# Performance work log

Measured on AMD Instinct MI355X. Metric: run time of the kernel, lower is better.

The kernel has to match this reference:

```python
import jax, jax.numpy as jnp
import numpy as np

B, N, C = 4, 32768, 256
H, CH, M = 8, 64, 64  # heads, dim_head, slice_num
INNER = H * CH


def setup_inputs() -> dict:
    key = jax.random.key(0)
    ks = jax.random.split(key, 16)
    s = lambda fan_in: 1.0 / np.sqrt(fan_in)
    return {
        "x": jax.random.normal(ks[0], (B, N, C), jnp.float32),
        "x_cross": jax.random.normal(ks[1], (B, N, C), jnp.float32),
        "Wfx": jax.random.normal(ks[2], (C, INNER), jnp.float32) * s(C),
        "bfx": jnp.zeros((INNER,), jnp.float32),
        "Wx": jax.random.normal(ks[3], (C, INNER), jnp.float32) * s(C),
        "bx": jnp.zeros((INNER,), jnp.float32),
        "Wslice": jax.random.normal(ks[4], (CH, M), jnp.float32) * s(CH),
        "bslice": jnp.zeros((M,), jnp.float32),
        "temperature": jnp.ones((1, H, 1, 1), jnp.float32) * 0.5,
        "Wq": jax.random.normal(ks[5], (CH, CH), jnp.float32) * s(CH),
        "Wk": jax.random.normal(ks[6], (CH, CH), jnp.float32) * s(CH),
        "Wv": jax.random.normal(ks[7], (CH, CH), jnp.float32) * s(CH),
        "Wo": jax.random.normal(ks[8], (INNER, C), jnp.float32) * s(INNER),
        "bo": jnp.zeros((C,), jnp.float32),
    }


def _split_heads(y):
    # [B, N, H*CH] -> [B, H, N, CH]
    return y.reshape(B, N, H, CH).transpose(0, 2, 1, 3)


def _project_token(x, Wfx, bfx, Wx, bx, Wslice, bslice, temperature):
    fx_mid = _split_heads(x @ Wfx + bfx)  # bhnc
    x_mid = _split_heads(x @ Wx + bx)     # bhnc
    temp = jnp.clip(temperature, 0.1, 5.0)
    logits = (x_mid @ Wslice + bslice) / temp  # b h n M
    sw = jax.nn.softmax(logits, axis=-1)
    sw = sw / (sw.sum(axis=2, keepdims=True) + 1e-5)  # normalize over N per slice
    token = jnp.einsum('bhnc,bhng->bhgc', fx_mid, sw)  # b h M CH
    return token, sw


def reference(x, x_cross, Wfx, bfx, Wx, bx, Wslice, bslice, temperature,
              Wq, Wk, Wv, Wo, bo):
    token, sw = _project_token(x, Wfx, bfx, Wx, bx, Wslice, bslice, temperature)
    token_c, _ = _project_token(x_cross, Wfx, bfx, Wx, bx, Wslice, bslice, temperature)

    q = token @ Wq    # b h M CH
    k = token_c @ Wk
    v = token_c @ Wv
    scale = CH ** -0.5
    attn = jax.nn.softmax(jnp.einsum('bhgc,bhmc->bhgm', q, k) * scale, axis=-1)
    out_tok = jnp.einsum('bhgm,bhmc->bhgc', attn, v)  # b h M CH

    out_x = jnp.einsum('bhgc,bhng->bhnc', out_tok, sw)  # b h N CH
    out_x = out_x.transpose(0, 2, 1, 3).reshape(B, N, INNER)
    return out_x @ Wo + bo
```

## Files before the change

### kernel.cpp

```cpp
#include <hip/hip_runtime.h>
#include <math.h>

constexpr int Bc = 4, Nc = 32768, Cc = 256, Hc = 8, CHc = 64, Mc = 64, INNERc = 512;

typedef _Float16 h8 __attribute__((ext_vector_type(8)));
typedef _Float16 h4 __attribute__((ext_vector_type(4)));
typedef float f32x4 __attribute__((ext_vector_type(4)));

__device__ __forceinline__ void fma4x4(float acc[4][4], const float4 a, const float4 b) {
  acc[0][0] += a.x*b.x; acc[0][1] += a.x*b.y; acc[0][2] += a.x*b.z; acc[0][3] += a.x*b.w;
  acc[1][0] += a.y*b.x; acc[1][1] += a.y*b.y; acc[1][2] += a.y*b.z; acc[1][3] += a.y*b.w;
  acc[2][0] += a.z*b.x; acc[2][1] += a.z*b.y; acc[2][2] += a.z*b.z; acc[2][3] += a.z*b.w;
  acc[3][0] += a.w*b.x; acc[3][1] += a.w*b.y; acc[3][2] += a.w*b.z; acc[3][3] += a.w*b.w;
}

__global__ __launch_bounds__(256, 2)
void project_token_kernel(const float* __restrict__ Xx, const float* __restrict__ Xc,
                          const float* __restrict__ Wfx, const float* __restrict__ bfx,
                          const float* __restrict__ Wx, const float* __restrict__ bx,
                          const float* __restrict__ Wsl, const float* __restrict__ bsl,
                          const float* __restrict__ temp,
                          float* __restrict__ TUx, float* __restrict__ TUc,
                          float* __restrict__ Ssx, float* __restrict__ Ssc)
{
  __shared__ __align__(16) _Float16 Xst[2][2][64][40];
  __shared__ __align__(16) _Float16 FXT[2][64][72];
  __shared__ __align__(16) _Float16 XMT[2][64][72];
  __shared__ __align__(16) float Sred[16][64];

  const int t = threadIdx.x;
  const int chunk = blockIdx.x, h = blockIdx.y, bz = blockIdx.z;
  const int b = bz & 3;
  const float* X = (bz < 4) ? Xx : Xc;
  float* TU   = (bz < 4) ? TUx : TUc;
  float* Ssum = (bz < 4) ? Ssx : Ssc;
  const int bh = b * Hc + h, colBase = h * 64;
  const int w = t >> 6, l = t & 63, lg = l >> 4, lr = l & 15;
  const int stok = t >> 2, sc8 = (t & 3) << 3;

  const float invt = 1.0f / fminf(fmaxf(temp[h], 0.1f), 5.0f);

  const float* Wsrc = (w < 2) ? Wfx : Wx;
  const float* bsrc = (w < 2) ? bfx : bx;
  const int wcb = colBase + ((w & 1) << 5);
  h8 wfh[8][2], wfl[8][2];
  float biasv[2];
#pragma unroll
  for (int n = 0; n < 2; ++n) {
    const int col = wcb + (n << 4) + lr;
    biasv[n] = bsrc[col];
#pragma unroll
    for (int ks = 0; ks < 8; ++ks)
#pragma unroll
      for (int j = 0; j < 8; ++j) {
        const float v = Wsrc[(long)((ks << 5) + (lg << 3) + j) * INNERc + col];
        const _Float16 hi = (_Float16)v;
        wfh[ks][n][j] = hi;
        wfl[ks][n][j] = (_Float16)(v - (float)hi);
      }
  }
  h8 wslh[2][4], wsll[2][4];
#pragma unroll
  for (int ks = 0; ks < 2; ++ks)
#pragma unroll
    for (int n = 0; n < 4; ++n)
#pragma unroll
      for (int j = 0; j < 8; ++j) {
        const float v = Wsl[((ks << 5) + (lg << 3) + j) * 64 + (n << 4) + lr];
        const _Float16 hi = (_Float16)v;
        wslh[ks][n][j] = hi;
        wsll[ks][n][j] = (_Float16)(v - (float)hi);
      }
  float bs_n[4];
#pragma unroll
  for (int n = 0; n < 4; ++n) bs_n[n] = bsl[(n << 4) + lr];

  f32x4 tuacc[4] = {};
  float sregn[4] = {};

  for (int tile = 0; tile < 32; ++tile) {
    const int n0 = chunk * 2048 + tile * 64;
    const long xRow = ((long)(b * Nc + n0 + stok)) * Cc + sc8;

    f32x4 acc[4][2] = {};
    {
      const float4 xa = *(const float4*)&X[xRow];
      const float4 xb = *(const float4*)&X[xRow + 4];
      const float va[8] = {xa.x, xa.y, xa.z, xa.w, xb.x, xb.y, xb.z, xb.w};
      h8 hv, lv;
#pragma unroll
      for (int j = 0; j < 8; ++j) {
        const _Float16 hi = (_Float16)va[j];
        hv[j] = hi; lv[j] = (_Float16)(va[j] - (float)hi);
      }
      *(h8*)&Xst[0][0][stok][sc8] = hv;
      *(h8*)&Xst[0][1][stok][sc8] = lv;
    }
#pragma unroll
    for (int ks = 0; ks < 8; ++ks) {
      const int cb = ks & 1;
      __syncthreads();
      float4 xa, xb;
      if (ks < 7) {
        xa = *(const float4*)&X[xRow + ((ks + 1) << 5)];
        xb = *(const float4*)&X[xRow + ((ks + 1) << 5) + 4];
      }
#pragma unroll
      for (int m = 0; m < 4; ++m) {
        const h8 ah = *(const h8*)&Xst[cb][0][(m << 4) + lr][lg << 3];
        const h8 al = *(const h8*)&Xst[cb][1][(m << 4) + lr][lg << 3];
#pragma unroll
        for (int n = 0; n < 2; ++n) {
          acc[m][n] = __builtin_amdgcn_mfma_f32_16x16x32_f16(ah, wfh[ks][n], acc[m][n], 0, 0, 0);
          acc[m][n] = __builtin_amdgcn_mfma_f32_16x16x32_f16(al, wfh[ks][n], acc[m][n], 0, 0, 0);
          acc[m][n] = __builtin_amdgcn_mfma_f32_16x16x32_f16(ah, wfl[ks][n], acc[m][n], 0, 0, 0);
        }
      }
      if (ks < 7) {
        const float va[8] = {xa.x, xa.y, xa.z, xa.w, xb.x, xb.y, xb.z, xb.w};
        h8 hv, lv;
#pragma unroll
        for (int j = 0; j < 8; ++j) {
          const _Float16 hi = (_Float16)va[j];
          hv[j] = hi; lv[j] = (_Float16)(va[j] - (float)hi);
        }
        *(h8*)&Xst[cb ^ 1][0][stok][sc8] = hv;
        *(h8*)&Xst[cb ^ 1][1][stok][sc8] = lv;
      }
    }

    if (w < 2) {
#pragma unroll
      for (int m = 0; m < 4; ++m)
#pragma unroll
        for (int n = 0; n < 2; ++n) {
          const int c = ((w & 1) << 5) + (n << 4) + lr;
          const int tokb = (m << 4) + (lg << 2);
          h4 hv, lv;
#pragma unroll
          for (int i = 0; i < 4; ++i) {
            const float v = acc[m][n][i] + biasv[n];
            const _Float16 hi = (_Float16)v;
            hv[i] = hi; lv[i] = (_Float16)(v - (float)hi);
          }
          *(h4*)&FXT[0][c][tokb] = hv;
          *(h4*)&FXT[1][c][tokb] = lv;
        }
    } else {
#pragma unroll
      for (int m = 0; m < 4; ++m)
#pragma unroll
        for (int n = 0; n < 2; ++n) {
          const int c = ((w & 1) << 5) + (n << 4) + lr;
#pragma unroll
          for (int i = 0; i < 4; ++i) {
            const float v = acc[m][n][i] + biasv[n];
            const _Float16 hi = (_Float16)v;
            XMT[0][(m << 4) + (lg << 2) + i][c] = hi;
            XMT[1][(m << 4) + (lg << 2) + i][c] = (_Float16)(v - (float)hi);
          }
        }
    }
    __syncthreads();

    f32x4 lga[4] = {};
#pragma unroll
    for (int ks = 0; ks < 2; ++ks) {
      const h8 ah = *(const h8*)&XMT[0][(w << 4) + lr][(ks << 5) + (lg << 3)];
      const h8 al = *(const h8*)&XMT[1][(w << 4) + lr][(ks << 5) + (lg << 3)];
#pragma unroll
      for (int n = 0; n < 4; ++n) {
        lga[n] = __builtin_amdgcn_mfma_f32_16x16x32_f16(ah, wslh[ks][n], lga[n], 0, 0, 0);
        lga[n] = __builtin_amdgcn_mfma_f32_16x16x32_f16(al, wslh[ks][n], lga[n], 0, 0, 0);
        lga[n] = __builtin_amdgcn_mfma_f32_16x16x32_f16(ah, wsll[ks][n], lga[n], 0, 0, 0);
      }
    }
    __syncthreads();

    float sw[4][4];
#pragma unroll
    for (int i = 0; i < 4; ++i) {
      float mx = -1e30f;
#pragma unroll
      for (int n = 0; n < 4; ++n) {
        const float lv = (lga[n][i] + bs_n[n]) * invt;
        sw[n][i] = lv; mx = fmaxf(mx, lv);
      }
      for (int d = 1; d < 16; d <<= 1) mx = fmaxf(mx, __shfl_xor(mx, d));
      float s = 0.f;
#pragma unroll
      for (int n = 0; n < 4; ++n) { sw[n][i] = __expf(sw[n][i] - mx); s += sw[n][i]; }
      for (int d = 1; d < 16; d <<= 1) s += __shfl_xor(s, d);
      const float inv = 1.0f / s;
#pragma unroll
      for (int n = 0; n < 4; ++n) { sw[n][i] *= inv; sregn[n] += sw[n][i]; }
    }
#pragma unroll
    for (int n = 0; n < 4; ++n) {
      h4 hv, lv;
#pragma unroll
      for (int i = 0; i < 4; ++i) {
        const _Float16 hi = (_Float16)sw[n][i];
        hv[i] = hi; lv[i] = (_Float16)(sw[n][i] - (float)hi);
      }
      *(h4*)&XMT[0][(n << 4) + lr][(w << 4) + (lg << 2)] = hv;
      *(h4*)&XMT[1][(n << 4) + lr][(w << 4) + (lg << 2)] = lv;
    }
    __syncthreads();

#pragma unroll
    for (int ks = 0; ks < 2; ++ks) {
      const h8 ah = *(const h8*)&XMT[0][(w << 4) + lr][(ks << 5) + (lg << 3)];
      const h8 al = *(const h8*)&XMT[1][(w << 4) + lr][(ks << 5) + (lg << 3)];
#pragma unroll
      for (int n = 0; n < 4; ++n) {
        const h8 bhv = *(const h8*)&FXT[0][(n << 4) + lr][(ks << 5) + (lg << 3)];
        const h8 blv = *(const h8*)&FXT[1][(n << 4) + lr][(ks << 5) + (lg << 3)];
        tuacc[n] = __builtin_amdgcn_mfma_f32_16x16x32_f16(ah, bhv, tuacc[n], 0, 0, 0);
        tuacc[n] = __builtin_amdgcn_mfma_f32_16x16x32_f16(al, bhv, tuacc[n], 0, 0, 0);
        tuacc[n] = __builtin_amdgcn_mfma_f32_16x16x32_f16(ah, blv, tuacc[n], 0, 0, 0);
      }
    }
  }

#pragma unroll
  for (int n = 0; n < 4; ++n)
#pragma unroll
    for (int i = 0; i < 4; ++i)
      atomicAdd(&TU[((long)bh * 64 + (w << 4) + (lg << 2) + i) * 64 + (n << 4) + lr],
                tuacc[n][i]);

  __syncthreads();
#pragma unroll
  for (int n = 0; n < 4; ++n) Sred[(w << 2) + lg][(n << 4) + lr] = sregn[n];
  __syncthreads();
  if (t < 64) {
    float s = 0.f;
    for (int r = 0; r < 16; ++r) s += Sred[r][t];
    atomicAdd(&Ssum[bh * 64 + t], s);
  }
}

__global__ __launch_bounds__(64)
void att_kernel(const float* __restrict__ TUx, const float* __restrict__ TUc,
                const float* __restrict__ Sx, const float* __restrict__ Sc,
                const float* __restrict__ Wq, const float* __restrict__ Wk,
                const float* __restrict__ Wv, float* __restrict__ OT)
{
  __shared__ __align__(16) float W[64][68];
  __shared__ __align__(16) float Km[64][68];
  __shared__ __align__(16) float Vm[64][68];
  const int bh = blockIdx.x;
  const int g  = threadIdx.x;
  const float invc = 1.0f / (Sc[bh * 64 + g] + 1e-5f);
  const float invx = 1.0f / (Sx[bh * 64 + g] + 1e-5f);

  for (int i = 0; i < 64; ++i) W[i][g] = Wk[i * 64 + g];
  __syncthreads();
  {
    float4 a[16]; for (int j = 0; j < 16; ++j) a[j] = make_float4(0,0,0,0);
    for (int c = 0; c < 64; ++c) {
      const float tc = TUc[((long)bh * 64 + g) * 64 + c] * invc;
#pragma unroll
      for (int j = 0; j < 16; ++j) {
        const float4 w4 = *(const float4*)&W[c][j << 2];
        a[j].x += tc*w4.x; a[j].y += tc*w4.y; a[j].z += tc*w4.z; a[j].w += tc*w4.w;
      }
    }
    for (int j = 0; j < 16; ++j) *(float4*)&Km[g][j << 2] = a[j];
  }
  __syncthreads();
  for (int i = 0; i < 64; ++i) W[i][g] = Wv[i * 64 + g];
  __syncthreads();
  {
    float4 a[16]; for (int j = 0; j < 16; ++j) a[j] = make_float4(0,0,0,0);
    for (int c = 0; c < 64; ++c) {
      const float tc = TUc[((long)bh * 64 + g) * 64 + c] * invc;
#pragma unroll
      for (int j = 0; j < 16; ++j) {
        const float4 w4 = *(const float4*)&W[c][j << 2];
        a[j].x += tc*w4.x; a[j].y += tc*w4.y; a[j].z += tc*w4.z; a[j].w += tc*w4.w;
      }
    }
    for (int j = 0; j < 16; ++j) *(float4*)&Vm[g][j << 2] = a[j];
  }
  __syncthreads();
  for (int i = 0; i < 64; ++i) W[i][g] = Wq[i * 64 + g];
  __syncthreads();
  float4 qa[16]; for (int j = 0; j < 16; ++j) qa[j] = make_float4(0,0,0,0);
  for (int c = 0; c < 64; ++c) {
    const float tq = TUx[((long)bh * 64 + g) * 64 + c] * invx;
#pragma unroll
    for (int j = 0; j < 16; ++j) {
      const float4 w4 = *(const float4*)&W[c][j << 2];
      qa[j].x += tq*w4.x; qa[j].y += tq*w4.y; qa[j].z += tq*w4.z; qa[j].w += tq*w4.w;
    }
  }
  __syncthreads();
  float (*Am)[68] = W;
  float mx = -1e30f;
  for (int m = 0; m < 64; ++m) {
    float s = 0.f;
#pragma unroll
    for (int j = 0; j < 16; ++j) {
      const float4 k4 = *(const float4*)&Km[m][j << 2];
      s += qa[j].x*k4.x + qa[j].y*k4.y + qa[j].z*k4.z + qa[j].w*k4.w;
    }
    s *= 0.125f;
    Am[m][g] = s;
    mx = fmaxf(mx, s);
  }
  float sum = 0.f;
  for (int m = 0; m < 64; ++m) { const float ev = __expf(Am[m][g] - mx); Am[m][g] = ev; sum += ev; }
  float4 oa[16]; for (int j = 0; j < 16; ++j) oa[j] = make_float4(0,0,0,0);
  for (int m = 0; m < 64; ++m) {
    const float am = Am[m][g];
#pragma unroll
    for (int j = 0; j < 16; ++j) {
      const float4 v4 = *(const float4*)&Vm[m][j << 2];
      oa[j].x += am*v4.x; oa[j].y += am*v4.y; oa[j].z += am*v4.z; oa[j].w += am*v4.w;
    }
  }
  const float so = invx / sum;
#pragma unroll
  for (int j = 0; j < 16; ++j) {
    OT[((long)bh * 64 + ((j<<2)+0)) * 64 + g] = oa[j].x * so;
    OT[((long)bh * 64 + ((j<<2)+1)) * 64 + g] = oa[j].y * so;
    OT[((long)bh * 64 + ((j<<2)+2)) * 64 + g] = oa[j].z * so;
    OT[((long)bh * 64 + ((j<<2)+3)) * 64 + g] = oa[j].w * so;
  }
}

__global__ __launch_bounds__(256)
void wofold_kernel(const float* __restrict__ OT, const float* __restrict__ Wo,
                   _Float16* __restrict__ WoTth, _Float16* __restrict__ WoTtl)
{
  __shared__ __align__(16) float OTs[64][68];
  __shared__ __align__(16) float Wos[64][68];
  const int t = threadIdx.x, tx = t & 15, ty = t >> 4;
  const int cot = blockIdx.x * 64, bh = blockIdx.y, h = bh & 7;
#pragma unroll
  for (int rep = 0; rep < 4; ++rep) {
    const int v = t + rep * 256, r = v >> 4, q4 = (v & 15) << 2;
    *(float4*)&OTs[r][q4] = *(const float4*)&OT[((long)bh * 64 + r) * 64 + q4];
    *(float4*)&Wos[r][q4] = *(const float4*)&Wo[(long)(h * 64 + r) * 256 + cot + q4];
  }
  __syncthreads();
  float acc[4][4] = {};
#pragma unroll
  for (int k = 0; k < 64; ++k) {
    const float4 a = *(const float4*)&OTs[k][ty << 2];
    fma4x4(acc, a, *(const float4*)&Wos[k][tx << 2]);
  }
#pragma unroll
  for (int i = 0; i < 4; ++i)
#pragma unroll
    for (int j = 0; j < 4; ++j) {
      const float v = acc[i][j];
      const _Float16 hi = (_Float16)v;
      const long o = ((long)bh * 256 + cot + (tx<<2)+j) * 64 + (ty<<2)+i;
      WoTth[o] = hi;
      WoTtl[o] = (_Float16)(v - (float)hi);
    }
}

__global__ __launch_bounds__(256)
void wxprep_kernel(const float* __restrict__ Wx, _Float16* __restrict__ Wxth,
                   _Float16* __restrict__ Wxtl)
{
  __shared__ __align__(16) float Ls[64][68];
  const int t = threadIdx.x;
  const int k0 = blockIdx.x * 64, c0 = blockIdx.y * 64;
  const int r = t >> 4, c4 = (t & 15) << 2;
#pragma unroll
  for (int rr = 0; rr < 4; ++rr)
    *(float4*)&Ls[(rr<<4)+r][c4] = *(const float4*)&Wx[(long)(k0+(rr<<4)+r) * 512 + c0 + c4];
  __syncthreads();
  const int cl = t >> 2, kq = (t & 3) << 4;
  h8 hv0, hv1, lv0, lv1;
#pragma unroll
  for (int kk = 0; kk < 8; ++kk) {
    float v = Ls[kq+kk][cl];
    _Float16 hi = (_Float16)v;
    hv0[kk] = hi; lv0[kk] = (_Float16)(v - (float)hi);
    v = Ls[kq+8+kk][cl];
    hi = (_Float16)v;
    hv1[kk] = hi; lv1[kk] = (_Float16)(v - (float)hi);
  }
  const long o = (long)(c0 + cl) * 256 + k0 + kq;
  *(h8*)&Wxth[o]     = hv0; *(h8*)&Wxth[o + 8] = hv1;
  *(h8*)&Wxtl[o]     = lv0; *(h8*)&Wxtl[o + 8] = lv1;
}

__global__ __launch_bounds__(256, 1)
void outx_kernel(const float* __restrict__ X, const _Float16* __restrict__ Wxth,
                 const _Float16* __restrict__ Wxtl, const float* __restrict__ bx,
                 const float* __restrict__ Wsl, const float* __restrict__ bsl,
                 const float* __restrict__ temp,
                 const _Float16* __restrict__ WoTth, const _Float16* __restrict__ WoTtl,
                 const float* __restrict__ bo, float* __restrict__ out)
{
  __shared__ __align__(16) _Float16 Xh[64][264];
  __shared__ __align__(16) _Float16 Xl[64][264];
  __shared__ __align__(16) _Float16 XMh[64][72];
  __shared__ __align__(16) _Float16 XMl[64][72];
  __shared__ __align__(16) float    Lg[64][68];

  const int t = threadIdx.x, tx = t & 15, ty = t >> 4;
  const int w = t >> 6, l = t & 63, lg = l >> 4, lr = l & 15;
  const int n0 = blockIdx.x * 64, b = blockIdx.y;
  const long xBase = ((long)b * Nc + n0) * Cc;

#pragma unroll
  for (int q = 0; q < 16; ++q) {
    const int row = (q << 2) + w, col = l << 2;
    const float4 v = *(const float4*)&X[xBase + (long)row * 256 + col];
    const float va[4] = {v.x, v.y, v.z, v.w};
    h4 hv, lv;
#pragma unroll
    for (int jj = 0; jj < 4; ++jj) {
      const _Float16 hi = (_Float16)va[jj];
      hv[jj] = hi; lv[jj] = (_Float16)(va[jj] - (float)hi);
    }
    *(h4*)&Xh[row][col] = hv;
    *(h4*)&Xl[row][col] = lv;
  }

  h8 wslh[2], wsll[2];
#pragma unroll
  for (int ks = 0; ks < 2; ++ks)
#pragma unroll
    for (int j = 0; j < 8; ++j) {
      const float v = Wsl[((ks << 5) + (lg << 3) + j) * 64 + (w << 4) + lr];
      const _Float16 hi = (_Float16)v;
      wslh[ks][j] = hi; wsll[ks][j] = (_Float16)(v - (float)hi);
    }
  const float bslv = bsl[(w << 4) + lr];

  f32x4 oacc[4][4] = {};

  __syncthreads();

  for (int h = 0; h < Hc; ++h) {
    h8 wxh[8], wxl[8];
    const long wxoff = (long)((h << 6) + (w << 4) + lr) * 256 + (lg << 3);
#pragma unroll
    for (int ks = 0; ks < 8; ++ks) {
      wxh[ks] = *(const h8*)&Wxth[wxoff + (ks << 5)];
      wxl[ks] = *(const h8*)&Wxtl[wxoff + (ks << 5)];
    }
    const float bxv = bx[(h << 6) + (w << 4) + lr];
    const float invt = 1.0f / fminf(fmaxf(temp[h], 0.1f), 5.0f);

    f32x4 xma[4] = {};
#pragma unroll
    for (int ks = 0; ks < 8; ++ks) {
#pragma unroll
      for (int m = 0; m < 4; ++m) {
        const h8 ah = *(const h8*)&Xh[(m << 4) + lr][(ks << 5) + (lg << 3)];
        const h8 al = *(const h8*)&Xl[(m << 4) + lr][(ks << 5) + (lg << 3)];
        xma[m] = __builtin_amdgcn_mfma_f32_16x16x32_f16(ah, wxh[ks], xma[m], 0, 0, 0);
        xma[m] = __builtin_amdgcn_mfma_f32_16x16x32_f16(al, wxh[ks], xma[m], 0, 0, 0);
        xma[m] = __builtin_amdgcn_mfma_f32_16x16x32_f16(ah, wxl[ks], xma[m], 0, 0, 0);
      }
    }
#pragma unroll
    for (int m = 0; m < 4; ++m)
#pragma unroll
      for (int i = 0; i < 4; ++i) {
        const float v = xma[m][i] + bxv;
        const _Float16 hi = (_Float16)v;
        XMh[(m << 4) + (lg << 2) + i][(w << 4) + lr] = hi;
        XMl[(m << 4) + (lg << 2) + i][(w << 4) + lr] = (_Float16)(v - (float)hi);
      }
    __syncthreads();

    const int bh = (b << 3) + h;
    h8 wth[4][2], wtl[4][2];
#pragma unroll
    for (int n = 0; n < 4; ++n)
#pragma unroll
      for (int ks = 0; ks < 2; ++ks) {
        const long o = ((long)(bh << 8) + (w << 6) + (n << 4) + lr) * 64 + (ks << 5) + (lg << 3);
        wth[n][ks] = *(const h8*)&WoTth[o];
        wtl[n][ks] = *(const h8*)&WoTtl[o];
      }

    f32x4 lga[4] = {};
#pragma unroll
    for (int ks = 0; ks < 2; ++ks)
#pragma unroll
      for (int m = 0; m < 4; ++m) {
        const h8 ah = *(const h8*)&XMh[(m << 4) + lr][(ks << 5) + (lg << 3)];
        const h8 al = *(const h8*)&XMl[(m << 4) + lr][(ks << 5) + (lg << 3)];
        lga[m] = __builtin_amdgcn_mfma_f32_16x16x32_f16(ah, wslh[ks], lga[m], 0, 0, 0);
        lga[m] = __builtin_amdgcn_mfma_f32_16x16x32_f16(al, wslh[ks], lga[m], 0, 0, 0);
        lga[m] = __builtin_amdgcn_mfma_f32_16x16x32_f16(ah, wsll[ks], lga[m], 0, 0, 0);
      }
#pragma unroll
    for (int m = 0; m < 4; ++m)
#pragma unroll
      for (int i = 0; i < 4; ++i)
        Lg[(m << 4) + (lg << 2) + i][(w << 4) + lr] = (lga[m][i] + bslv) * invt;
    __syncthreads();

    float e[4][4];
#pragma unroll
    for (int i = 0; i < 4; ++i) {
      const float4 lv4 = *(const float4*)&Lg[(ty << 2) + i][tx << 2];
      const float lrow[4] = {lv4.x, lv4.y, lv4.z, lv4.w};
      float mx = fmaxf(fmaxf(lrow[0], lrow[1]), fmaxf(lrow[2], lrow[3]));
      for (int d = 1; d < 16; d <<= 1) mx = fmaxf(mx, __shfl_xor(mx, d));
      float s = 0.f;
#pragma unroll
      for (int j = 0; j < 4; ++j) { e[i][j] = __expf(lrow[j] - mx); s += e[i][j]; }
      for (int d = 1; d < 16; d <<= 1) s += __shfl_xor(s, d);
      const float inv = 1.0f / s;
#pragma unroll
      for (int j = 0; j < 4; ++j) e[i][j] *= inv;
    }
#pragma unroll
    for (int i = 0; i < 4; ++i)
#pragma unroll
      for (int j = 0; j < 4; ++j) {
        const _Float16 hi = (_Float16)e[i][j];
        XMh[(ty << 2) + i][(tx << 2) + j] = hi;
        XMl[(ty << 2) + i][(tx << 2) + j] = (_Float16)(e[i][j] - (float)hi);
      }
    __syncthreads();

#pragma unroll
    for (int ks = 0; ks < 2; ++ks)
#pragma unroll
      for (int m = 0; m < 4; ++m) {
        const h8 ah = *(const h8*)&XMh[(m << 4) + lr][(ks << 5) + (lg << 3)];
        const h8 al = *(const h8*)&XMl[(m << 4) + lr][(ks << 5) + (lg << 3)];
#pragma unroll
        for (int n = 0; n < 4; ++n) {
          oacc[m][n] = __builtin_amdgcn_mfma_f32_16x16x32_f16(ah, wth[n][ks], oacc[m][n], 0, 0, 0);
          oacc[m][n] = __builtin_amdgcn_mfma_f32_16x16x32_f16(al, wth[n][ks], oacc[m][n], 0, 0, 0);
          oacc[m][n] = __builtin_amdgcn_mfma_f32_16x16x32_f16(ah, wtl[n][ks], oacc[m][n], 0, 0, 0);
        }
      }
    __syncthreads();
  }

#pragma unroll
  for (int n = 0; n < 4; ++n) {
    const float bov = bo[(w << 6) + (n << 4) + lr];
#pragma unroll
    for (int m = 0; m < 4; ++m)
#pragma unroll
      for (int i = 0; i < 4; ++i)
        out[((long)b * Nc + n0 + (m << 4) + (lg << 2) + i) * 256 + (w << 6) + (n << 4) + lr]
            = oacc[m][n][i] + bov;
  }
}

extern "C" void kernel_launch(void* const* d_in, const int* in_sizes, int n_in,
                              void* d_out, int out_size, void* d_ws, size_t ws_size,
                              hipStream_t stream)
{
  (void)in_sizes; (void)n_in; (void)out_size; (void)ws_size;
  const float* x    = (const float*)d_in[0];
  const float* xc   = (const float*)d_in[1];
  const float* Wfx  = (const float*)d_in[2];
  const float* bfx  = (const float*)d_in[3];
  const float* Wx   = (const float*)d_in[4];
  const float* bx   = (const float*)d_in[5];
  const float* Wsl  = (const float*)d_in[6];
  const float* bsl  = (const float*)d_in[7];
  const float* temp = (const float*)d_in[8];
  const float* Wq   = (const float*)d_in[9];
  const float* Wk   = (const float*)d_in[10];
  const float* Wv   = (const float*)d_in[11];
  const float* Wo   = (const float*)d_in[12];
  const float* bo   = (const float*)d_in[13];
  float* out = (float*)d_out;

  float* ws  = (float*)d_ws;
  float* Sx  = ws;
  float* Sc  = Sx + 2048;
  float* TUx = Sc + 2048;
  float* TUc = TUx + 131072;
  float* OT  = TUc + 131072;
  _Float16* WoTth = (_Float16*)(OT + 131072);
  _Float16* WoTtl = WoTth + 524288;
  _Float16* Wxth  = WoTtl + 524288;
  _Float16* Wxtl  = Wxth + 131072;

  hipMemsetAsync(Sx, 0, (size_t)(2 * 2048 + 2 * 131072) * sizeof(float), stream);

  wxprep_kernel<<<dim3(4, 8), 256, 0, stream>>>(Wx, Wxth, Wxtl);
  project_token_kernel<<<dim3(16, 8, 8), 256, 0, stream>>>(
      x, xc, Wfx, bfx, Wx, bx, Wsl, bsl, temp, TUx, TUc, Sx, Sc);
  att_kernel<<<dim3(32), dim3(64), 0, stream>>>(TUx, TUc, Sx, Sc, Wq, Wk, Wv, OT);
  wofold_kernel<<<dim3(4, 32), 256, 0, stream>>>(OT, Wo, WoTth, WoTtl);
  outx_kernel<<<dim3(512, 4), 256, 0, stream>>>(x, Wxth, Wxtl, bx, Wsl, bsl, temp, WoTth, WoTtl, bo, out);
}
```

Measured before the change: 1.551 ms.

## Precompute fp16 hi/lo planes of inputs and restructure outx softmax in registers

A new pre-pass splits x and x_cross into interleaved fp16 hi/lo planes. The x planes are stored in the output buffer as scratch, and the x_cross planes go into the workspace when it is large enough. project_token and outx then feed MFMA operands straight from these planes in global memory, instead of converting fp32 and staging through LDS on every pass. outx also keeps the slice logits and softmax in registers, dropping the Lg and X shared buffers, and asks for two blocks per CU. The cost is an extra full read/write pass over the inputs. It also relies on outx reading each block's own rows of out before overwriting them.

Result: slower. 2.727 ms (+75.8%).

```diff
diff --git a/kernel.cpp b/kernel.cpp
--- a/kernel.cpp
+++ b/kernel.cpp
@@ -14,8 +14,27 @@
   acc[3][0] += a.w*b.x; acc[3][1] += a.w*b.y; acc[3][2] += a.w*b.z; acc[3][3] += a.w*b.w;
 }
 
+__global__ __launch_bounds__(256)
+void xplanes_kernel(const float* __restrict__ src, _Float16* __restrict__ dst)
+{
+  const long idx = (long)blockIdx.x * 256 + threadIdx.x;
+  const long row = idx >> 5, oc = idx & 31;
+  const float4 a = *(const float4*)&src[(row << 8) + (oc << 3)];
+  const float4 b = *(const float4*)&src[(row << 8) + (oc << 3) + 4];
+  const float va[8] = {a.x, a.y, a.z, a.w, b.x, b.y, b.z, b.w};
+  h8 hv, lv;
+#pragma unroll
+  for (int j = 0; j < 8; ++j) {
+    const _Float16 hi = (_Float16)va[j];
+    hv[j] = hi; lv[j] = (_Float16)(va[j] - (float)hi);
+  }
+  *(h8*)&dst[(row << 9) + (oc << 4)]     = hv;
+  *(h8*)&dst[(row << 9) + (oc << 4) + 8] = lv;
+}
+
 __global__ __launch_bounds__(256, 2)
 void project_token_kernel(const float* __restrict__ Xx, const float* __restrict__ Xc,
+                          const _Float16* __restrict__ Xix, const _Float16* __restrict__ Xic,
                           const float* __restrict__ Wfx, const float* __restrict__ bfx,
                           const float* __restrict__ Wx, const float* __restrict__ bx,
                           const float* __restrict__ Wsl, const float* __restrict__ bsl,
@@ -26,12 +45,13 @@
   __shared__ __align__(16) _Float16 Xst[2][2][64][40];
   __shared__ __align__(16) _Float16 FXT[2][64][72];
   __shared__ __align__(16) _Float16 XMT[2][64][72];
-  __shared__ __align__(16) float Sred[16][64];
+  float (*Sred)[64] = (float(*)[64])&Xst[0][0][0][0];
 
   const int t = threadIdx.x;
   const int chunk = blockIdx.x, h = blockIdx.y, bz = blockIdx.z;
   const int b = bz & 3;
   const float* X = (bz < 4) ? Xx : Xc;
+  const _Float16* Xi = (bz < 4) ? Xix : Xic;
   float* TU   = (bz < 4) ? TUx : TUc;
   float* Ssum = (bz < 4) ? Ssx : Ssc;
   const int bh = b * Hc + h, colBase = h * 64;
@@ -80,43 +100,30 @@
 
   for (int tile = 0; tile < 32; ++tile) {
     const int n0 = chunk * 2048 + tile * 64;
-    const long xRow = ((long)(b * Nc + n0 + stok)) * Cc + sc8;
-
     f32x4 acc[4][2] = {};
-    {
-      const float4 xa = *(const float4*)&X[xRow];
-      const float4 xb = *(const float4*)&X[xRow + 4];
-      const float va[8] = {xa.x, xa.y, xa.z, xa.w, xb.x, xb.y, xb.z, xb.w};
-      h8 hv, lv;
-#pragma unroll
-      for (int j = 0; j < 8; ++j) {
-        const _Float16 hi = (_Float16)va[j];
-        hv[j] = hi; lv[j] = (_Float16)(va[j] - (float)hi);
-      }
-      *(h8*)&Xst[0][0][stok][sc8] = hv;
-      *(h8*)&Xst[0][1][stok][sc8] = lv;
-    }
-#pragma unroll
-    for (int ks = 0; ks < 8; ++ks) {
-      const int cb = ks & 1;
+
+    if (Xi) {
       __syncthreads();
-      float4 xa, xb;
-      if (ks < 7) {
-        xa = *(const float4*)&X[xRow + ((ks + 1) << 5)];
-        xb = *(const float4*)&X[xRow + ((ks + 1) << 5) + 4];
-      }
-#pragma unroll
-      for (int m = 0; m < 4; ++m) {
-        const h8 ah = *(const h8*)&Xst[cb][0][(m << 4) + lr][lg << 3];
-        const h8 al = *(const h8*)&Xst[cb][1][(m << 4) + lr][lg << 3];
-#pragma unroll
-        for (int n = 0; n < 2; ++n) {
-          acc[m][n] = __builtin_amdgcn_mfma_f32_16x16x32_f16(ah, wfh[ks][n], acc[m][n], 0, 0, 0);
-          acc[m][n] = __builtin_amdgcn_mfma_f32_16x16x32_f16(al, wfh[ks][n], acc[m][n], 0, 0, 0);
-          acc[m][n] = __builtin_amdgcn_mfma_f32_16x16x32_f16(ah, wfl[ks][n], acc[m][n], 0, 0, 0);
-        }
-      }
-      if (ks < 7) {
+      const long rbase = ((long)(b * Nc + n0)) * 512;
+#pragma unroll
+      for (int ks = 0; ks < 8; ++ks) {
+#pragma unroll
+        for (int m = 0; m < 4; ++m) {
+          const h8* p = (const h8*)&Xi[rbase + (long)((m << 4) + lr) * 512 + (((ks << 2) + lg) << 4)];
+          const h8 ah = p[0], al = p[1];
+#pragma unroll
+          for (int n = 0; n < 2; ++n) {
+            acc[m][n] = __builtin_amdgcn_mfma_f32_16x16x32_f16(ah, wfh[ks][n], acc[m][n], 0, 0, 0);
+            acc[m][n] = __builtin_amdgcn_mfma_f32_16x16x32_f16(al, wfh[ks][n], acc[m][n], 0, 0, 0);
+            acc[m][n] = __builtin_amdgcn_mfma_f32_16x16x32_f16(ah, wfl[ks][n], acc[m][n], 0, 0, 0);
+          }
+        }
+      }
+    } else {
+      const long xRow = ((long)(b * Nc + n0 + stok)) * Cc + sc8;
+      {
+        const float4 xa = *(const float4*)&X[xRow];
+        const float4 xb = *(const float4*)&X[xRow + 4];
         const float va[8] = {xa.x, xa.y, xa.z, xa.w, xb.x, xb.y, xb.z, xb.w};
         h8 hv, lv;
 #pragma unroll
@@ -124,8 +131,40 @@
           const _Float16 hi = (_Float16)va[j];
           hv[j] = hi; lv[j] = (_Float16)(va[j] - (float)hi);
         }
-        *(h8*)&Xst[cb ^ 1][0][stok][sc8] = hv;
-        *(h8*)&Xst[cb ^ 1][1][stok][sc8] = lv;
+        *(h8*)&Xst[0][0][stok][sc8] = hv;
+        *(h8*)&Xst[0][1][stok][sc8] = lv;
+      }
+#pragma unroll
+      for (int ks = 0; ks < 8; ++ks) {
+        const int cb = ks & 1;
+        __syncthreads();
+        float4 xa, xb;
+        if (ks < 7) {
+          xa = *(const float4*)&X[xRow + ((ks + 1) << 5)];
+          xb = *(const float4*)&X[xRow + ((ks + 1) << 5) + 4];
+        }
+#pragma unroll
+        for (int m = 0; m < 4; ++m) {
+          const h8 ah = *(const h8*)&Xst[cb][0][(m << 4) + lr][lg << 3];
+          const h8 al = *(const h8*)&Xst[cb][1][(m << 4) + lr][lg << 3];
+#pragma unroll
+          for (int n = 0; n < 2; ++n) {
+            acc[m][n] = __builtin_amdgcn_mfma_f32_16x16x32_f16(ah, wfh[ks][n], acc[m][n], 0, 0, 0);
+            acc[m][n] = __builtin_amdgcn_mfma_f32_16x16x32_f16(al, wfh[ks][n], acc[m][n], 0, 0, 0);
+            acc[m][n] = __builtin_amdgcn_mfma_f32_16x16x32_f16(ah, wfl[ks][n], acc[m][n], 0, 0, 0);
+          }
+        }
+        if (ks < 7) {
+          const float va[8] = {xa.x, xa.y, xa.z, xa.w, xb.x, xb.y, xb.z, xb.w};
+          h8 hv, lv;
+#pragma unroll
+          for (int j = 0; j < 8; ++j) {
+            const _Float16 hi = (_Float16)va[j];
+            hv[j] = hi; lv[j] = (_Float16)(va[j] - (float)hi);
+          }
+          *(h8*)&Xst[cb ^ 1][0][stok][sc8] = hv;
+          *(h8*)&Xst[cb ^ 1][1][stok][sc8] = lv;
+        }
       }
     }
 
@@ -392,54 +431,37 @@
   *(h8*)&Wxtl[o]     = lv0; *(h8*)&Wxtl[o + 8] = lv1;
 }
 
-__global__ __launch_bounds__(256, 1)
-void outx_kernel(const float* __restrict__ X, const _Float16* __restrict__ Wxth,
+__global__ __launch_bounds__(256, 2)
+void outx_kernel(const _Float16* Xi, const _Float16* __restrict__ Wxth,
                  const _Float16* __restrict__ Wxtl, const float* __restrict__ bx,
                  const float* __restrict__ Wsl, const float* __restrict__ bsl,
                  const float* __restrict__ temp,
                  const _Float16* __restrict__ WoTth, const _Float16* __restrict__ WoTtl,
-                 const float* __restrict__ bo, float* __restrict__ out)
+                 const float* __restrict__ bo, float* out)
 {
-  __shared__ __align__(16) _Float16 Xh[64][264];
-  __shared__ __align__(16) _Float16 Xl[64][264];
-  __shared__ __align__(16) _Float16 XMh[64][72];
-  __shared__ __align__(16) _Float16 XMl[64][72];
-  __shared__ __align__(16) float    Lg[64][68];
-
-  const int t = threadIdx.x, tx = t & 15, ty = t >> 4;
+  __shared__ __align__(16) _Float16 XMT[2][64][72];
+
+  const int t = threadIdx.x;
   const int w = t >> 6, l = t & 63, lg = l >> 4, lr = l & 15;
   const int n0 = blockIdx.x * 64, b = blockIdx.y;
-  const long xBase = ((long)b * Nc + n0) * Cc;
-
-#pragma unroll
-  for (int q = 0; q < 16; ++q) {
-    const int row = (q << 2) + w, col = l << 2;
-    const float4 v = *(const float4*)&X[xBase + (long)row * 256 + col];
-    const float va[4] = {v.x, v.y, v.z, v.w};
-    h4 hv, lv;
-#pragma unroll
-    for (int jj = 0; jj < 4; ++jj) {
-      const _Float16 hi = (_Float16)va[jj];
-      hv[jj] = hi; lv[jj] = (_Float16)(va[jj] - (float)hi);
-    }
-    *(h4*)&Xh[row][col] = hv;
-    *(h4*)&Xl[row][col] = lv;
-  }
-
-  h8 wslh[2], wsll[2];
+  const long rbase = ((long)b * Nc + n0) * 512;
+
+  h8 wslh[2][4], wsll[2][4];
 #pragma unroll
   for (int ks = 0; ks < 2; ++ks)
 #pragma unroll
-    for (int j = 0; j < 8; ++j) {
-      const float v = Wsl[((ks << 5) + (lg << 3) + j) * 64 + (w << 4) + lr];
-      const _Float16 hi = (_Float16)v;
-      wslh[ks][j] = hi; wsll[ks][j] = (_Float16)(v - (float)hi);
-    }
-  const float bslv = bsl[(w << 4) + lr];
+    for (int n = 0; n < 4; ++n)
+#pragma unroll
+      for (int j = 0; j < 8; ++j) {
+        const float v = Wsl[((ks << 5) + (lg << 3) + j) * 64 + (n << 4) + lr];
+        const _Float16 hi = (_Float16)v;
+        wslh[ks][n][j] = hi; wsll[ks][n][j] = (_Float16)(v - (float)hi);
+      }
+  float bs_n[4];
+#pragma unroll
+  for (int n = 0; n < 4; ++n) bs_n[n] = bsl[(n << 4) + lr];
 
   f32x4 oacc[4][4] = {};
-
-  __syncthreads();
 
   for (int h = 0; h < Hc; ++h) {
     h8 wxh[8], wxl[8];
@@ -457,21 +479,22 @@
     for (int ks = 0; ks < 8; ++ks) {
 #pragma unroll
       for (int m = 0; m < 4; ++m) {
-        const h8 ah = *(const h8*)&Xh[(m << 4) + lr][(ks << 5) + (lg << 3)];
-        const h8 al = *(const h8*)&Xl[(m << 4) + lr][(ks << 5) + (lg << 3)];
+        const h8* p = (const h8*)&Xi[rbase + (long)((m << 4) + lr) * 512 + (((ks << 2) + lg) << 4)];
+        const h8 ah = p[0], al = p[1];
         xma[m] = __builtin_amdgcn_mfma_f32_16x16x32_f16(ah, wxh[ks], xma[m], 0, 0, 0);
         xma[m] = __builtin_amdgcn_mfma_f32_16x16x32_f16(al, wxh[ks], xma[m], 0, 0, 0);
         xma[m] = __builtin_amdgcn_mfma_f32_16x16x32_f16(ah, wxl[ks], xma[m], 0, 0, 0);
       }
     }
+    __syncthreads();
 #pragma unroll
     for (int m = 0; m < 4; ++m)
 #pragma unroll
       for (int i = 0; i < 4; ++i) {
         const float v = xma[m][i] + bxv;
         const _Float16 hi = (_Float16)v;
-        XMh[(m << 4) + (lg << 2) + i][(w << 4) + lr] = hi;
-        XMl[(m << 4) + (lg << 2) + i][(w << 4) + lr] = (_Float16)(v - (float)hi);
+        XMT[0][(m << 4) + (lg << 2) + i][(w << 4) + lr] = hi;
+        XMT[1][(m << 4) + (lg << 2) + i][(w << 4) + lr] = (_Float16)(v - (float)hi);
       }
     __syncthreads();
 
@@ -488,44 +511,43 @@
 
     f32x4 lga[4] = {};
 #pragma unroll
-    for (int ks = 0; ks < 2; ++ks)
-#pragma unroll
-      for (int m = 0; m < 4; ++m) {
-        const h8 ah = *(const h8*)&XMh[(m << 4) + lr][(ks << 5) + (lg << 3)];
-        const h8 al = *(const h8*)&XMl[(m << 4) + lr][(ks << 5) + (lg << 3)];
-        lga[m] = __builtin_amdgcn_mfma_f32_16x16x32_f16(ah, wslh[ks], lga[m], 0, 0, 0);
-        lga[m] = __builtin_amdgcn_mfma_f32_16x16x32_f16(al, wslh[ks], lga[m], 0, 0, 0);
-        lga[m] = __builtin_amdgcn_mfma_f32_16x16x32_f16(ah, wsll[ks], lga[m], 0, 0, 0);
-      }
-#pragma unroll
-    for (int m = 0; m < 4; ++m)
-#pragma unroll
-      for (int i = 0; i < 4; ++i)
-        Lg[(m << 4) + (lg << 2) + i][(w << 4) + lr] = (lga[m][i] + bslv) * invt;
+    for (int ks = 0; ks < 2; ++ks) {
+      const h8 ah = *(const h8*)&XMT[0][(w << 4) + lr][(ks << 5) + (lg << 3)];
+      const h8 al = *(const h8*)&XMT[1][(w << 4) + lr][(ks << 5) + (lg << 3)];
+#pragma unroll
+      for (int n = 0; n < 4; ++n) {
+        lga[n] = __builtin_amdgcn_mfma_f32_16x16x32_f16(ah, wslh[ks][n], lga[n], 0, 0, 0);
+        lga[n] = __builtin_amdgcn_mfma_f32_16x16x32_f16(al, wslh[ks][n], lga[n], 0, 0, 0);
+        lga[n] = __builtin_amdgcn_mfma_f32_16x16x32_f16(ah, wsll[ks][n], lga[n], 0, 0, 0);
+      }
+    }
     __syncthreads();
 
-    float e[4][4];
+    float sw[4][4];
 #pragma unroll
     for (int i = 0; i < 4; ++i) {
-      const float4 lv4 = *(const float4*)&Lg[(ty << 2) + i][tx << 2];
-      const float lrow[4] = {lv4.x, lv4.y, lv4.z, lv4.w};
-      float mx = fmaxf(fmaxf(lrow[0], lrow[1]), fmaxf(lrow[2], lrow[3]));
+      float mx = -1e30f;
+#pragma unroll
+      for (int n = 0; n < 4; ++n) {
+        const float lv = (lga[n][i] + bs_n[n]) * invt;
+        sw[n][i] = lv; mx = fmaxf(mx, lv);
+      }
       for (int d = 1; d < 16; d <<= 1) mx = fmaxf(mx, __shfl_xor(mx, d));
       float s = 0.f;
 #pragma unroll
-      for (int j = 0; j < 4; ++j) { e[i][j] = __expf(lrow[j] - mx); s += e[i][j]; }
+      for (int n = 0; n < 4; ++n) { sw[n][i] = __expf(sw[n][i] - mx); s += sw[n][i]; }
       for (int d = 1; d < 16; d <<= 1) s += __shfl_xor(s, d);
       const float inv = 1.0f / s;
 #pragma unroll
-      for (int j = 0; j < 4; ++j) e[i][j] *= inv;
-    }
-#pragma unroll
-    for (int i = 0; i < 4; ++i)
-#pragma unroll
-      for (int j = 0; j < 4; ++j) {
-        const _Float16 hi = (_Float16)e[i][j];
-        XMh[(ty << 2) + i][(tx << 2) + j] = hi;
-        XMl[(ty << 2) + i][(tx << 2) + j] = (_Float16)(e[i][j] - (float)hi);
+      for (int n = 0; n < 4; ++n) sw[n][i] *= inv;
+    }
+#pragma unroll
+    for (int n = 0; n < 4; ++n)
+#pragma unroll
+      for (int i = 0; i < 4; ++i) {
+        const _Float16 hi = (_Float16)sw[n][i];
+        XMT[0][(w << 4) + (lg << 2) + i][(n << 4) + lr] = hi;
+        XMT[1][(w << 4) + (lg << 2) + i][(n << 4) + lr] = (_Float16)(sw[n][i] - (float)hi);
       }
     __syncthreads();
 
@@ -533,8 +555,8 @@
     for (int ks = 0; ks < 2; ++ks)
 #pragma unroll
       for (int m = 0; m < 4; ++m) {
-        const h8 ah = *(const h8*)&XMh[(m << 4) + lr][(ks << 5) + (lg << 3)];
-        const h8 al = *(const h8*)&XMl[(m << 4) + lr][(ks << 5) + (lg << 3)];
+        const h8 ah = *(const h8*)&XMT[0][(m << 4) + lr][(ks << 5) + (lg << 3)];
+        const h8 al = *(const h8*)&XMT[1][(m << 4) + lr][(ks << 5) + (lg << 3)];
 #pragma unroll
         for (int n = 0; n < 4; ++n) {
           oacc[m][n] = __builtin_amdgcn_mfma_f32_16x16x32_f16(ah, wth[n][ks], oacc[m][n], 0, 0, 0);
@@ -542,7 +564,6 @@
           oacc[m][n] = __builtin_amdgcn_mfma_f32_16x16x32_f16(ah, wtl[n][ks], oacc[m][n], 0, 0, 0);
         }
       }
-    __syncthreads();
   }
 
 #pragma unroll
@@ -561,7 +582,7 @@
                               void* d_out, int out_size, void* d_ws, size_t ws_size,
                               hipStream_t stream)
 {
-  (void)in_sizes; (void)n_in; (void)out_size; (void)ws_size;
+  (void)in_sizes; (void)n_in; (void)out_size;
   const float* x    = (const float*)d_in[0];
   const float* xc   = (const float*)d_in[1];
   const float* Wfx  = (const float*)d_in[2];
@@ -588,13 +609,24 @@
   _Float16* WoTtl = WoTth + 524288;
   _Float16* Wxth  = WoTtl + 524288;
   _Float16* Wxtl  = Wxth + 131072;
+  _Float16* Xic   = Wxtl + 131072;
+
+  const size_t baseBytes = (size_t)((char*)Xic - (char*)d_ws);
+  const size_t planeBytes = (size_t)Bc * Nc * 512 * sizeof(_Float16);
+  const bool xcFits = ws_size >= baseBytes + planeBytes;
+
+  _Float16* XiOut = (_Float16*)d_out;
 
   hipMemsetAsync(Sx, 0, (size_t)(2 * 2048 + 2 * 131072) * sizeof(float), stream);
 
+  xplanes_kernel<<<dim3(16384), 256, 0, stream>>>(x, XiOut);
+  if (xcFits) xplanes_kernel<<<dim3(16384), 256, 0, stream>>>(xc, Xic);
   wxprep_kernel<<<dim3(4, 8), 256, 0, stream>>>(Wx, Wxth, Wxtl);
   project_token_kernel<<<dim3(16, 8, 8), 256, 0, stream>>>(
-      x, xc, Wfx, bfx, Wx, bx, Wsl, bsl, temp, TUx, TUc, Sx, Sc);
+      x, xc, XiOut, xcFits ? Xic : (const _Float16*)nullptr,
+      Wfx, bfx, Wx, bx, Wsl, bsl, temp, TUx, TUc, Sx, Sc);
   att_kernel<<<dim3(32), dim3(64), 0, stream>>>(TUx, TUc, Sx, Sc, Wq, Wk, Wv, OT);
   wofold_kernel<<<dim3(4, 32), 256, 0, stream>>>(OT, Wo, WoTth, WoTtl);
-  outx_kernel<<<dim3(512, 4), 256, 0, stream>>>(x, Wxth, Wxtl, bx, Wsl, bsl, temp, WoTth, WoTtl, bo, out);
-}
+  outx_kernel<<<dim3(512, 4), 256, 0, stream>>>(XiOut, Wxth, Wxtl, bx, Wsl, bsl, temp,
+                                                WoTth, WoTtl, bo, out);
+}
```
